# Optimization experiments

Hardware: AMD Instinct MI355X
Metric: run time of the kernel (lower is better)

The kernel has to match this reference:

```python
import jax, jax.numpy as jnp
import numpy as np

B, T, IN, H, OUT = 32, 512, 50, 512, 66
DIGITS = 5          # total_digits -> 6 softmax blocks of width 11
EPS = 0.01          # ACT halting threshold epsilon
MAX_PONDER = 10     # max ponder steps per timestep (fixed for jit)


def setup_inputs() -> dict:
    key = jax.random.key(0)
    ks = jax.random.split(key, 6)
    s_in = 1.0 / np.sqrt(IN + 1)
    s_h = 1.0 / np.sqrt(H)
    return {
        "x": jax.random.normal(ks[0], (B, T, IN), jnp.float32),
        # LSTM cell over input augmented with the ACT first-step flag (IN+1)
        "W_ih": jax.random.normal(ks[1], (4 * H, IN + 1), jnp.float32) * s_in,
        "W_hh": jax.random.normal(ks[2], (4 * H, H), jnp.float32) * s_h,
        "b": jnp.zeros((4 * H,), jnp.float32),
        "W_out": jax.random.normal(ks[3], (OUT, H), jnp.float32) * s_h,
        "b_out": jnp.zeros((OUT,), jnp.float32),
        "W_halt": jax.random.normal(ks[4], (H,), jnp.float32) * s_h,
        "b_halt": jnp.ones((), jnp.float32),
    }


def _lstm_cell(x_aug, h, c, W_ih, W_hh, b):
    g = x_aug @ W_ih.T + h @ W_hh.T + b          # [B, 4H]
    i, f, gg, o = jnp.split(g, 4, axis=-1)
    c = jax.nn.sigmoid(f) * c + jax.nn.sigmoid(i) * jnp.tanh(gg)
    h = jax.nn.sigmoid(o) * jnp.tanh(c)
    return h, c


def _act_lstm(x, W_ih, W_hh, b, W_out, b_out, W_halt, b_halt):
    Bb, Tt, _ = x.shape
    h0 = jnp.zeros((Bb, H), x.dtype)
    c0 = jnp.zeros((Bb, H), x.dtype)

    def time_step(carry, x_t):
        h, c = carry

        def ponder_step(pc, n):
            ph, pcell, cum, acc_h, acc_c, acc_y, n_upd, rem, done = pc
            flag = jnp.where(n == 0, 1.0, 0.0).astype(x_t.dtype)
            x_aug = jnp.concatenate(
                [x_t, jnp.broadcast_to(flag, (Bb, 1))], axis=-1)
            h2, c2 = _lstm_cell(x_aug, ph, pcell, W_ih, W_hh, b)
            y = h2 @ W_out.T + b_out                    # [B, OUT]
            halt = jax.nn.sigmoid(h2 @ W_halt + b_halt)  # [B]
            is_last = n == (MAX_PONDER - 1)
            halted = ((cum + halt) > (1.0 - EPS)) | is_last
            p = jnp.where(done, 0.0, jnp.where(halted, 1.0 - cum, halt))
            acc_h = acc_h + p[:, None] * h2
            acc_c = acc_c + p[:, None] * c2
            acc_y = acc_y + p[:, None] * y
            n_upd = n_upd + jnp.where(done, 0.0, 1.0)
            rem = rem + jnp.where(done | ~halted, 0.0, 1.0 - cum)
            cum = cum + jnp.where(done, 0.0, halt)
            done = done | halted
            return (h2, c2, cum, acc_h, acc_c, acc_y, n_upd, rem, done), None

        zb = jnp.zeros((Bb,), x.dtype)
        init = (h, c, zb,
                jnp.zeros((Bb, H), x.dtype), jnp.zeros((Bb, H), x.dtype),
                jnp.zeros((Bb, OUT), x.dtype), zb, zb,
                jnp.zeros((Bb,), bool))
        (_, _, _, wh, wc, wy, n_upd, rem, _), _ = jax.lax.scan(
            ponder_step, init, jnp.arange(MAX_PONDER))
        return (wh, wc), (wy, n_upd + rem)

    _, (ys, p) = jax.lax.scan(time_step, (h0, c0), jnp.swapaxes(x, 0, 1))
    out = jnp.swapaxes(ys, 0, 1)   # [B, T, OUT]
    p = jnp.swapaxes(p, 0, 1)      # [B, T] ponder cost
    return out, p


def reference(x, W_ih, W_hh, b, W_out, b_out, W_halt, b_halt):
    out, p = _act_lstm(x, W_ih, W_hh, b, W_out, b_out, W_halt, b_halt)
    Bb, Tt, _ = out.shape
    # per-segment softmax: 6 blocks of width 11 along the feature axis
    out = jax.nn.softmax(out.reshape(Bb, Tt, DIGITS + 1, 11), axis=-1)
    out = out.reshape(Bb, Tt, OUT)
    return out, p
```

## Files before the change

### kernel.cpp

```cpp
#include <hip/hip_runtime.h>
#include <stdint.h>
#include <stddef.h>


#define NBLK 256

#define WS_NEED_BYTES 38434816ull

__device__ __forceinline__ float sigmf(float v) { return 1.0f / (1.0f + expf(-v)); }

__device__ __forceinline__ void store_llc(float* p, float v) {
  asm volatile("global_store_dword %0, %1, off sc0 sc1" :: "v"(p), "v"(v) : "memory");
}
__device__ __forceinline__ void store_llc_u(unsigned* p, unsigned v) {
  asm volatile("global_store_dword %0, %1, off sc0 sc1" :: "v"(p), "v"(v) : "memory");
}
__device__ __forceinline__ unsigned load_llc_u(const unsigned* p) {
  unsigned v;
  asm volatile("global_load_dword %0, %1, off sc0 sc1\ns_waitcnt vmcnt(0)"
               : "=&v"(v) : "v"(p) : "memory");
  return v;
}

#if defined(__has_builtin)
#if __has_builtin(__builtin_amdgcn_global_load_lds)
#define HAVE_GLLDS 1
#endif
#endif

__device__ __forceinline__ void stage_instr(const float* gp, float* lp) {
#ifdef HAVE_GLLDS
  __builtin_amdgcn_global_load_lds((const __attribute__((address_space(1))) unsigned int*)gp,
                                   (__attribute__((address_space(3))) unsigned int*)lp,
                                   16, 0, 0x11);
#else
  float4 tmp;
  asm volatile("global_load_dwordx4 %0, %1, off sc0 sc1" : "=v"(tmp) : "v"(gp) : "memory");
  asm volatile("s_waitcnt vmcnt(0)" ::: "memory");
  *(float4*)(lp + (threadIdx.x & 63) * 4) = tmp;
#endif
}

__global__ void prep_k(const float* __restrict__ W_ih, const float* __restrict__ W_hh,
                       const float* __restrict__ W_out,
                       float* __restrict__ Wp, float* __restrict__ W_iT,
                       float* __restrict__ W_oT, unsigned* __restrict__ bar) {
  int idx = blockIdx.x * 256 + threadIdx.x;
  if (idx < 1048576) {
    int kl = idx & 3, c = (idx >> 2) & 63, k4 = (idx >> 8) & 127, r = idx >> 15;
    int row = (c & 3) * 512 + 16 * r + (c >> 2);
    Wp[idx] = W_hh[(size_t)row * 512 + 4 * k4 + kl];
  }
  int i2 = idx - 1048576;
  if (i2 >= 0 && i2 < 104448) {
    int col = i2 & 2047, k = i2 >> 11;
    int g = col & 3, j = col >> 2;
    W_iT[i2] = W_ih[(size_t)((g << 9) + j) * 51 + k];
  }
  int i3 = idx - 1153024;
  if (i3 >= 0 && i3 < 33792) {
    int k = i3 / 66, o = i3 - k * 66;
    W_oT[i3] = W_out[(size_t)o * 512 + k];
  }
  int i4 = idx - 1186816;
  if (i4 >= 0 && i4 < 512) bar[i4] = 0u;
}

__global__ void __launch_bounds__(256)
act_main(const float* __restrict__ x, const float* __restrict__ bvec,
         const float* __restrict__ W_halt, const float* __restrict__ b_halt,
         const float* __restrict__ Wp, const float* __restrict__ W_iT,
         float* __restrict__ hbuf, unsigned* __restrict__ bar,
         float* __restrict__ wh, float* __restrict__ p_out) {
  extern __shared__ __align__(16) float wl[];
  __shared__ float hst[2048];
  __shared__ float pacc[1024];
  __shared__ float xg2[256];
  __shared__ float hps[256];
  __shared__ float S_p[4];
  __shared__ int S_flag[1];

  const int tid = threadIdx.x, bid = blockIdx.x;
  const int gid = bid >> 5, r = bid & 31;
  const int c = tid & 63, w = tid >> 6, lane = tid & 63;
  const int jj = tid >> 2, bo = tid & 3;
  const int ch = lane >> 2, b2 = lane & 3;
  unsigned* flags = bar + gid * 32;
  float* hbG = hbuf + gid * 4096;

  {
    const float* wsrc = Wp + (size_t)r * 32768;
    for (int i = tid; i < 8192; i += 256)
      *(float4*)(wl + i * 4) = *(const float4*)(wsrc + i * 4);
  }

  const float bh = b_halt[0];
  const int cg = 64 * r + c;
  const float bs = bvec[(c & 3) * 512 + 16 * r + (c >> 2)];
  const float wfc = W_iT[50 * 2048 + cg];

  float gAcc = 0.f, gxc, gxn = 0.f;
  {
    gxc = bs;
    const float* xr = x + (size_t)(gid * 4 + w) * 512 * 50;
    for (int k = 0; k < 50; ++k) gxc = fmaf(xr[k], W_iT[k * 2048 + cg], gxc);
  }
  float cS = 0.f, hprev = 0.f, acc_h = 0.f, acc_c = 0.f;
  float cum = 0.f, nupd = 0.f, rem = 0.f;
  int mydone = 0;

  int t = 0, n = 0, first = 1;
  unsigned ph = 0;
  long pollbud = 8000000L;
  __syncthreads();

  while (true) {
    float val, cin = 0.f;
    if (first) {
      val = gxc + wfc;
      first = 0;
    } else {
      {
        const unsigned* fp = flags + w * 8 + (lane & 7);
        while (true) {
          unsigned fv = 0u;
          if (lane < 8) fv = load_llc_u(fp);
          if (__ballot((lane < 8) ? (fv >= ph) : 1) == ~0ull) break;
          if (--pollbud < 0) break;
          __builtin_amdgcn_s_sleep(1);
        }
      }
      {
        const float* gp = hbG + ((ph & 1u) ^ 1u) * 2048 + w * 512 + lane * 4;
        float* lp = hst + w * 512;
        stage_instr(gp, lp); stage_instr(gp + 256, lp + 256);
      }
      if (n == 0) {
        const int tn = (t + 1 > 511) ? 511 : t + 1;
        gxn = bs;
        const float* xr = x + ((size_t)(gid * 4 + w) * 512 + tn) * 50;
        for (int k = 0; k < 50; ++k) gxn = fmaf(xr[k], W_iT[k * 2048 + cg], gxn);
      }
      asm volatile("s_waitcnt vmcnt(0)" ::: "memory");

      {
        const float* wb = wl + w * 8192 + c * 4;
        const float* hb = hst + w * 512;
        float a0 = 0.f, a1 = 0.f, a2 = 0.f, a3 = 0.f;
        #pragma unroll 8
        for (int i = 0; i < 32; ++i) {
          const float4 wv = *(const float4*)(wb + i * 256);
          const float4 h0 = *(const float4*)(hb + i * 16);
          const float4 h1 = *(const float4*)(hb + i * 16 + 4);
          const float4 h2v = *(const float4*)(hb + i * 16 + 8);
          const float4 h3 = *(const float4*)(hb + i * 16 + 12);
          a0 = fmaf(wv.x, h0.x, a0); a1 = fmaf(wv.x, h0.y, a1);
          a2 = fmaf(wv.x, h0.z, a2); a3 = fmaf(wv.x, h0.w, a3);
          a0 = fmaf(wv.y, h1.x, a0); a1 = fmaf(wv.y, h1.y, a1);
          a2 = fmaf(wv.y, h1.z, a2); a3 = fmaf(wv.y, h1.w, a3);
          a0 = fmaf(wv.z, h2v.x, a0); a1 = fmaf(wv.z, h2v.y, a1);
          a2 = fmaf(wv.z, h2v.z, a2); a3 = fmaf(wv.z, h2v.w, a3);
          a0 = fmaf(wv.w, h3.x, a0); a1 = fmaf(wv.w, h3.y, a1);
          a2 = fmaf(wv.w, h3.z, a2); a3 = fmaf(wv.w, h3.w, a3);
        }
        float4 pv; pv.x = a0; pv.y = a1; pv.z = a2; pv.w = a3;
        *(float4*)(pacc + w * 256 + c * 4) = pv;
      }
      {
        float hp = 0.f;
        #pragma unroll
        for (int i = 0; i < 8; ++i) {
          const int k = 128 * w + ch + 16 * i;
          hp = fmaf(hst[k * 4 + b2], W_halt[k], hp);
        }
        hps[tid] = hp;
      }
      __syncthreads();

      const float g = pacc[c * 4 + w] + pacc[256 + c * 4 + w] +
                      pacc[512 + c * 4 + w] + pacc[768 + c * 4 + w];
      if (tid < 64) {
        int vote = 1;
        if (tid < 4) {
          float d = 0.f;
          for (int m = 0; m < 64; ++m) d += hps[m * 4 + tid];
          const float halt = sigmf(d + bh);
          const int done = mydone;
          const int halted = ((cum + halt) > 0.99f) || (n == 9);
          S_p[tid] = done ? 0.f : (halted ? (1.f - cum) : halt);
          nupd += done ? 0.f : 1.f;
          rem += (done || !halted) ? 0.f : (1.f - cum);
          cum += done ? 0.f : halt;
          mydone = done | halted;
          vote = mydone;
        }
        const unsigned long long bal = __ballot(vote);
        if (tid == 0) S_flag[0] = (bal == ~0ull) ? 1 : 0;
      }
      __syncthreads();

      const int alldone = S_flag[0];
      const float p = S_p[w];
      gAcc = fmaf(p, g, gAcc);
      if (tid < 64) {
        const float po = S_p[bo];
        acc_h = fmaf(po, hprev, acc_h);
        acc_c = fmaf(po, cS, acc_c);
      }
      if (alldone) {
        if (tid < 64) {
          wh[(size_t)t * 16384 + (size_t)(gid * 4 + bo) * 512 + 16 * r + jj] = acc_h;
          cin = acc_c;
          acc_h = 0.f; acc_c = 0.f;
        }
        if (r == 0 && tid < 4)
          p_out[(size_t)(gid * 4 + tid) * 512 + t] = nupd + rem;
        if (tid < 4) { cum = 0.f; nupd = 0.f; rem = 0.f; mydone = 0; }
        val = gxn + wfc + gAcc;
        gAcc = 0.f; gxc = gxn;
        t += 1; n = 0;
        if (t == 512) break;
      } else {
        if (tid < 64) cin = cS;
        val = gxc + g;
        n += 1;
      }
    }

    xg2[c * 4 + w] = val;
    __syncthreads();
    if (tid < 64) {
      const float gi = xg2[16 * jj + 0 + bo];
      const float gf = xg2[16 * jj + 4 + bo];
      const float gg = xg2[16 * jj + 8 + bo];
      const float go = xg2[16 * jj + 12 + bo];
      const float c_new = sigmf(gf) * cin + sigmf(gi) * tanhf(gg);
      const float h_new = sigmf(go) * tanhf(c_new);
      cS = c_new; hprev = h_new;
      store_llc(hbG + (ph & 1u) * 2048 + 64 * r + tid, h_new);
      asm volatile("s_waitcnt vmcnt(0)" ::: "memory");
      if (tid == 0) store_llc_u(&flags[r], ph + 1u);
    }
    ph += 1;
  }
}

__global__ void __launch_bounds__(256)
epi_k(const float* __restrict__ wh, const float* __restrict__ W_oT,
      const float* __restrict__ b_out, float* __restrict__ out) {
  __shared__ float hl[4][512];
  __shared__ float yl[4][66];
  const int tid = threadIdx.x, pair = tid >> 6, lane = tid & 63;
  const int bt = blockIdx.x * 4 + pair;
  const int b = bt >> 9, t = bt & 511;
  const float* hsrc = wh + (size_t)t * 16384 + (size_t)b * 512;
  *(float4*)&hl[pair][lane * 8] = *(const float4*)(hsrc + lane * 8);
  *(float4*)&hl[pair][lane * 8 + 4] = *(const float4*)(hsrc + lane * 8 + 4);
  __syncthreads();
  if (lane < 33) {
    const int o = lane * 2;
    float y0 = b_out[o], y1 = b_out[o + 1];
    const float* hp_ = hl[pair];
    #pragma unroll 8
    for (int k = 0; k < 512; ++k) {
      const float h = hp_[k];
      const float2 wv = *(const float2*)(W_oT + k * 66 + o);
      y0 = fmaf(h, wv.x, y0);
      y1 = fmaf(h, wv.y, y1);
    }
    yl[pair][o] = y0; yl[pair][o + 1] = y1;
  }
  __syncthreads();
  if (tid < 24) {
    const int pr = tid / 6, g = tid - pr * 6;
    const int bt2 = blockIdx.x * 4 + pr;
    const float* yp = &yl[pr][g * 11];
    float m = yp[0];
    for (int u = 1; u < 11; ++u) m = fmaxf(m, yp[u]);
    float e[11], ssum = 0.f;
    for (int u = 0; u < 11; ++u) { e[u] = expf(yp[u] - m); ssum += e[u]; }
    const float inv = 1.0f / ssum;
    float* op = out + (size_t)bt2 * 66 + g * 11;
    for (int u = 0; u < 11; ++u) op[u] = e[u] * inv;
  }
}

extern "C" void kernel_launch(void* const* d_in, const int* in_sizes, int n_in,
                              void* d_out, int out_size, void* d_ws, size_t ws_size,
                              hipStream_t stream) {
  (void)in_sizes; (void)n_in; (void)out_size;
  const float* x      = (const float*)d_in[0];
  const float* W_ih   = (const float*)d_in[1];
  const float* W_hh   = (const float*)d_in[2];
  const float* bvec   = (const float*)d_in[3];
  const float* W_out  = (const float*)d_in[4];
  const float* b_out  = (const float*)d_in[5];
  const float* W_halt = (const float*)d_in[6];
  const float* b_halt = (const float*)d_in[7];
  float* out = (float*)d_out;
  float* ws  = (float*)d_ws;

  if (ws_size < (size_t)WS_NEED_BYTES) return;

  float* wh     = ws;
  float* hbuf   = ws + 8388608;
  unsigned* bar = (unsigned*)(ws + 8421376);
  float* Wp     = ws + 8421888;
  float* W_iT   = ws + 9470464;
  float* W_oT   = ws + 9574912;
  float* p_out  = out + 1081344;

  static int s_attr = 0;
  if (!s_attr) {
    (void)hipFuncSetAttribute((const void*)act_main,
                              hipFuncAttributeMaxDynamicSharedMemorySize, 131072);
    s_attr = 1;
  }

  hipLaunchKernelGGL(prep_k, dim3(4638), dim3(256), 0, stream,
                     W_ih, W_hh, W_out, Wp, W_iT, W_oT, bar);

  void* args[10];
  args[0] = (void*)&x;      args[1] = (void*)&bvec;  args[2] = (void*)&W_halt;
  args[3] = (void*)&b_halt; args[4] = (void*)&Wp;    args[5] = (void*)&W_iT;
  args[6] = (void*)&hbuf;   args[7] = (void*)&bar;   args[8] = (void*)&wh;
  args[9] = (void*)&p_out;
  hipError_t ce = hipLaunchCooperativeKernel((void*)act_main, dim3(NBLK), dim3(256),
                                             args, 131072, stream);
  if (ce != hipSuccess) {
    hipLaunchKernelGGL(act_main, dim3(NBLK), dim3(256), 131072, stream,
                       x, bvec, W_halt, b_halt, Wp, W_iT, hbuf, bar, wh, p_out);
  }

  hipLaunchKernelGGL(epi_k, dim3(4096), dim3(256), 0, stream, wh, W_oT, b_out, out);
}
```

Measured before the change: 8.651 ms.

## Embed step counters alongside h values in packed comm lines, drop separate flag barrier

Replaces the separate h buffer plus per-block flag array with a packed communication buffer. Each 16-float slot carries 15 h values and one phase counter, so a single store publishes data and readiness together. This removes the store→wait→flag-store round trip on the critical recurrence path, and readers poll the embedded counters directly before loading. It also turns the halt-logit reduction into a shuffle tree and moves W_out transposition after the main kernel so W_oT can reuse Wp's workspace. The cost is 40 polled loads per wave and scattered LDS writes, and it relies on 8-byte stores being observed atomically with their data.

```diff
diff --git a/kernel.cpp b/kernel.cpp
--- a/kernel.cpp
+++ b/kernel.cpp
@@ -9,12 +9,6 @@
 
 __device__ __forceinline__ float sigmf(float v) { return 1.0f / (1.0f + expf(-v)); }
 
-__device__ __forceinline__ void store_llc(float* p, float v) {
-  asm volatile("global_store_dword %0, %1, off sc0 sc1" :: "v"(p), "v"(v) : "memory");
-}
-__device__ __forceinline__ void store_llc_u(unsigned* p, unsigned v) {
-  asm volatile("global_store_dword %0, %1, off sc0 sc1" :: "v"(p), "v"(v) : "memory");
-}
 __device__ __forceinline__ unsigned load_llc_u(const unsigned* p) {
   unsigned v;
   asm volatile("global_load_dword %0, %1, off sc0 sc1\ns_waitcnt vmcnt(0)"
@@ -22,29 +16,9 @@
   return v;
 }
 
-#if defined(__has_builtin)
-#if __has_builtin(__builtin_amdgcn_global_load_lds)
-#define HAVE_GLLDS 1
-#endif
-#endif
-
-__device__ __forceinline__ void stage_instr(const float* gp, float* lp) {
-#ifdef HAVE_GLLDS
-  __builtin_amdgcn_global_load_lds((const __attribute__((address_space(1))) unsigned int*)gp,
-                                   (__attribute__((address_space(3))) unsigned int*)lp,
-                                   16, 0, 0x11);
-#else
-  float4 tmp;
-  asm volatile("global_load_dwordx4 %0, %1, off sc0 sc1" : "=v"(tmp) : "v"(gp) : "memory");
-  asm volatile("s_waitcnt vmcnt(0)" ::: "memory");
-  *(float4*)(lp + (threadIdx.x & 63) * 4) = tmp;
-#endif
-}
-
 __global__ void prep_k(const float* __restrict__ W_ih, const float* __restrict__ W_hh,
-                       const float* __restrict__ W_out,
                        float* __restrict__ Wp, float* __restrict__ W_iT,
-                       float* __restrict__ W_oT, unsigned* __restrict__ bar) {
+                       float* __restrict__ comm) {
   int idx = blockIdx.x * 256 + threadIdx.x;
   if (idx < 1048576) {
     int kl = idx & 3, c = (idx >> 2) & 63, k4 = (idx >> 8) & 127, r = idx >> 15;
@@ -58,25 +32,29 @@
     W_iT[i2] = W_ih[(size_t)((g << 9) + j) * 51 + k];
   }
   int i3 = idx - 1153024;
-  if (i3 >= 0 && i3 < 33792) {
-    int k = i3 / 66, o = i3 - k * 66;
-    W_oT[i3] = W_out[(size_t)o * 512 + k];
-  }
-  int i4 = idx - 1186816;
-  if (i4 >= 0 && i4 < 512) bar[i4] = 0u;
+  if (i3 >= 0 && i3 < 40960) comm[i3] = 0.0f;
+}
+
+__global__ void prep2_k(const float* __restrict__ W_out, float* __restrict__ W_oT) {
+  int i = blockIdx.x * 256 + threadIdx.x;
+  if (i < 33792) {
+    int k = i / 66, o = i - k * 66;
+    W_oT[i] = W_out[(size_t)o * 512 + k];
+  }
 }
 
 __global__ void __launch_bounds__(256)
 act_main(const float* __restrict__ x, const float* __restrict__ bvec,
          const float* __restrict__ W_halt, const float* __restrict__ b_halt,
          const float* __restrict__ Wp, const float* __restrict__ W_iT,
-         float* __restrict__ hbuf, unsigned* __restrict__ bar,
-         float* __restrict__ wh, float* __restrict__ p_out) {
+         float* __restrict__ comm, float* __restrict__ wh,
+         float* __restrict__ p_out) {
   extern __shared__ __align__(16) float wl[];
-  __shared__ float hst[2048];
+  __shared__ float hst[2052];
   __shared__ float pacc[1024];
   __shared__ float xg2[256];
   __shared__ float hps[256];
+  __shared__ float pubf[80];
   __shared__ float S_p[4];
   __shared__ int S_flag[1];
 
@@ -85,8 +63,6 @@
   const int c = tid & 63, w = tid >> 6, lane = tid & 63;
   const int jj = tid >> 2, bo = tid & 3;
   const int ch = lane >> 2, b2 = lane & 3;
-  unsigned* flags = bar + gid * 32;
-  float* hbG = hbuf + gid * 4096;
 
   {
     const float* wsrc = Wp + (size_t)r * 32768;
@@ -98,6 +74,23 @@
   const int cg = 64 * r + c;
   const float bs = bvec[(c & 3) * 512 + 16 * r + (c >> 2)];
   const float wfc = W_iT[50 * 2048 + cg];
+
+  const int pub_off = (tid / 15) * 16 + (tid % 15);
+  const int sp_off = (lane / 5) * 80 + (lane % 5) * 16 + 15;
+
+#define MKH(GW, DST) do { const int _q=(GW)/80, _o=(GW)%80, _li=_o>>4, _po=_o&15; \
+    const int _pi = _li*15 + _po; \
+    DST = ((_po < 15) && (_pi < 64)) ? (w*512 + _q*64 + _pi) : 2048; } while (0)
+  int hA0,hA1,hA2,hA3,hB0,hB1,hB2,hB3;
+  int hC0=2048,hC1=2048,hC2=2048,hC3=2048;
+  MKH(4*lane+0,hA0); MKH(4*lane+1,hA1); MKH(4*lane+2,hA2); MKH(4*lane+3,hA3);
+  MKH(256+4*lane+0,hB0); MKH(256+4*lane+1,hB1);
+  MKH(256+4*lane+2,hB2); MKH(256+4*lane+3,hB3);
+  if (lane < 32) {
+    MKH(512+4*lane+0,hC0); MKH(512+4*lane+1,hC1);
+    MKH(512+4*lane+2,hC2); MKH(512+4*lane+3,hC3);
+  }
+#undef MKH
 
   float gAcc = 0.f, gxc, gxn = 0.f;
   {
@@ -120,21 +113,26 @@
       val = gxc + wfc;
       first = 0;
     } else {
+      const unsigned par_rd = (ph & 1u) ^ 1u;
+      const float* cb = comm + (size_t)(par_rd * 256u + gid * 32 + 8 * w) * 80;
       {
-        const unsigned* fp = flags + w * 8 + (lane & 7);
+        const unsigned* stp = (const unsigned*)cb + sp_off;
         while (true) {
-          unsigned fv = 0u;
-          if (lane < 8) fv = load_llc_u(fp);
-          if (__ballot((lane < 8) ? (fv >= ph) : 1) == ~0ull) break;
+          unsigned sv = 0u;
+          if (lane < 40) sv = load_llc_u(stp);
+          if (__ballot((lane < 40) ? (sv >= ph) : 1) == ~0ull) break;
           if (--pollbud < 0) break;
           __builtin_amdgcn_s_sleep(1);
         }
       }
-      {
-        const float* gp = hbG + ((ph & 1u) ^ 1u) * 2048 + w * 512 + lane * 4;
-        float* lp = hst + w * 512;
-        stage_instr(gp, lp); stage_instr(gp + 256, lp + 256);
-      }
+      float4 vA, vB, vC;
+      asm volatile("global_load_dwordx4 %0, %1, off sc0 sc1"
+                   : "=v"(vA) : "v"(cb + 4 * lane) : "memory");
+      asm volatile("global_load_dwordx4 %0, %1, off sc0 sc1"
+                   : "=v"(vB) : "v"(cb + 256 + 4 * lane) : "memory");
+      if (lane < 32)
+        asm volatile("global_load_dwordx4 %0, %1, off sc0 sc1"
+                     : "=v"(vC) : "v"(cb + 512 + 4 * lane) : "memory");
       if (n == 0) {
         const int tn = (t + 1 > 511) ? 511 : t + 1;
         gxn = bs;
@@ -142,6 +140,11 @@
         for (int k = 0; k < 50; ++k) gxn = fmaf(xr[k], W_iT[k * 2048 + cg], gxn);
       }
       asm volatile("s_waitcnt vmcnt(0)" ::: "memory");
+      hst[hA0] = vA.x; hst[hA1] = vA.y; hst[hA2] = vA.z; hst[hA3] = vA.w;
+      hst[hB0] = vB.x; hst[hB1] = vB.y; hst[hB2] = vB.z; hst[hB3] = vB.w;
+      if (lane < 32) {
+        hst[hC0] = vC.x; hst[hC1] = vC.y; hst[hC2] = vC.z; hst[hC3] = vC.w;
+      }
 
       {
         const float* wb = wl + w * 8192 + c * 4;
@@ -180,11 +183,12 @@
       const float g = pacc[c * 4 + w] + pacc[256 + c * 4 + w] +
                       pacc[512 + c * 4 + w] + pacc[768 + c * 4 + w];
       if (tid < 64) {
+        float s = hps[tid] + hps[tid + 64] + hps[tid + 128] + hps[tid + 192];
+        s += __shfl_xor(s, 4);  s += __shfl_xor(s, 8);
+        s += __shfl_xor(s, 16); s += __shfl_xor(s, 32);
         int vote = 1;
         if (tid < 4) {
-          float d = 0.f;
-          for (int m = 0; m < 64; ++m) d += hps[m * 4 + tid];
-          const float halt = sigmf(d + bh);
+          const float halt = sigmf(s + bh);
           const int done = mydone;
           const int halted = ((cum + halt) > 0.99f) || (n == 9);
           S_p[tid] = done ? 0.f : (halted ? (1.f - cum) : halt);
@@ -237,9 +241,16 @@
       const float c_new = sigmf(gf) * cin + sigmf(gi) * tanhf(gg);
       const float h_new = sigmf(go) * tanhf(c_new);
       cS = c_new; hprev = h_new;
-      store_llc(hbG + (ph & 1u) * 2048 + 64 * r + tid, h_new);
-      asm volatile("s_waitcnt vmcnt(0)" ::: "memory");
-      if (tid == 0) store_llc_u(&flags[r], ph + 1u);
+      pubf[pub_off] = h_new;
+      if (tid < 5) pubf[tid * 16 + 15] = __uint_as_float(ph + 1u);
+    }
+    asm volatile("s_waitcnt lgkmcnt(0)" ::: "memory");
+    __builtin_amdgcn_sched_barrier(0);
+    if (tid < 40) {
+      const float2 pv = *(const float2*)&pubf[2 * tid];
+      float* cp = comm + (size_t)((ph & 1u) * 256u + gid * 32 + r) * 80 + 2 * tid;
+      asm volatile("global_store_dwordx2 %0, %1, off sc0 sc1"
+                   :: "v"(cp), "v"(pv) : "memory");
     }
     ph += 1;
   }
@@ -302,13 +313,12 @@
 
   if (ws_size < (size_t)WS_NEED_BYTES) return;
 
-  float* wh     = ws;
-  float* hbuf   = ws + 8388608;
-  unsigned* bar = (unsigned*)(ws + 8421376);
-  float* Wp     = ws + 8421888;
-  float* W_iT   = ws + 9470464;
-  float* W_oT   = ws + 9574912;
-  float* p_out  = out + 1081344;
+  float* wh   = ws;
+  float* comm = ws + 8388608;
+  float* Wp   = ws + 8429568;
+  float* W_iT = ws + 9478144;
+  float* W_oT = ws + 8429568;
+  float* p_out = out + 1081344;
 
   static int s_attr = 0;
   if (!s_attr) {
@@ -317,20 +327,20 @@
     s_attr = 1;
   }
 
-  hipLaunchKernelGGL(prep_k, dim3(4638), dim3(256), 0, stream,
-                     W_ih, W_hh, W_out, Wp, W_iT, W_oT, bar);
-
-  void* args[10];
+  hipLaunchKernelGGL(prep_k, dim3(4664), dim3(256), 0, stream,
+                     W_ih, W_hh, Wp, W_iT, comm);
+
+  void* args[9];
   args[0] = (void*)&x;      args[1] = (void*)&bvec;  args[2] = (void*)&W_halt;
   args[3] = (void*)&b_halt; args[4] = (void*)&Wp;    args[5] = (void*)&W_iT;
-  args[6] = (void*)&hbuf;   args[7] = (void*)&bar;   args[8] = (void*)&wh;
-  args[9] = (void*)&p_out;
+  args[6] = (void*)&comm;   args[7] = (void*)&wh;    args[8] = (void*)&p_out;
   hipError_t ce = hipLaunchCooperativeKernel((void*)act_main, dim3(NBLK), dim3(256),
                                              args, 131072, stream);
   if (ce != hipSuccess) {
     hipLaunchKernelGGL(act_main, dim3(NBLK), dim3(256), 131072, stream,
-                       x, bvec, W_halt, b_halt, Wp, W_iT, hbuf, bar, wh, p_out);
-  }
-
+                       x, bvec, W_halt, b_halt, Wp, W_iT, comm, wh, p_out);
+  }
+
+  hipLaunchKernelGGL(prep2_k, dim3(132), dim3(256), 0, stream, W_out, W_oT);
   hipLaunchKernelGGL(epi_k, dim3(4096), dim3(256), 0, stream, wh, W_oT, b_out, out);
 }
```

New measurement: 7.030 ms. 1.23x faster.
